# Kernel optimization log

Measured on AMD Instinct MI355X. Metric: run time of the kernel, lower is better.

Reference implementation:

```python
import jax, jax.numpy as jnp
import numpy as np
from jax import lax

NUM_SKETCH = 3
BN_EPS = 1e-5


def setup_inputs() -> dict:
    key = jax.random.key(0)
    ks = jax.random.split(key, 8)
    B, C, H, W = 32, 128, 64, 64
    D = C // 4  # comp_rate = 4
    k = 3
    x = jax.random.normal(ks[0], (B, C, H, W), dtype=jnp.float32)
    fan = C * k * k
    w1 = jax.random.normal(ks[1], (C, C, k, k), dtype=jnp.float32) / np.sqrt(fan)
    w2 = jax.random.normal(ks[2], (C, C, k, k), dtype=jnp.float32) / np.sqrt(fan)
    gamma1 = jnp.ones((C,), jnp.float32); beta1 = jnp.zeros((C,), jnp.float32)
    gamma2 = jnp.ones((C,), jnp.float32); beta2 = jnp.zeros((C,), jnp.float32)
    # count-sketch hash matrices: hs[j] is (D, C), each column c has a single 1
    idx = jax.random.randint(ks[3], (NUM_SKETCH, C), 0, D)
    hs = jax.nn.one_hot(idx, D, dtype=jnp.float32).transpose(0, 2, 1)  # (3, D, C)
    ss = (jax.random.randint(ks[4], (NUM_SKETCH, C), 0, 2) * 2 - 1).astype(jnp.float32)  # (3, C) signs
    return {"x": x, "w1": w1, "w2": w2, "gamma1": gamma1, "beta1": beta1,
            "gamma2": gamma2, "beta2": beta2, "hs": hs, "ss": ss}


def _sketch_conv_unsketch(x, w, hs, ss):
    # w: (Co, Ci, k, k); hs: (J, D, Co); ss: (J, Co)
    Co, Ci, k, _ = w.shape
    J, D, _ = hs.shape
    B, _, H, W = x.shape
    wf = w.reshape(Co, -1)  # (Co, M)
    # sketched weights per sketch j: h_j @ (wf * s_j[:, None])
    w_sk = jnp.einsum('jdc,jc,cm->jdm', hs, ss, wf).reshape(J * D, Ci, k, k)
    # one conv with J*D output channels (padding=1, stride=1 hardcoded in source)
    y = lax.conv_general_dilated(x, w_sk, window_strides=(1, 1),
                                 padding=[(1, 1), (1, 1)],
                                 dimension_numbers=('NCHW', 'OIHW', 'NCHW'))
    y = y.reshape(B, J, D, H, W)
    # unsketch activations: h_j^T @ y_j, then sign scale (num_s=1 so inner median is identity)
    y_un = jnp.einsum('jdc,bjdhw->jbchw', hs, y) * ss[:, None, :, None, None]
    return jnp.median(y_un, axis=0)  # median over the 3 sketches -> (B, Co, H, W)


def _bn_relu(y, gamma, beta):
    # BatchNorm2d in training mode: biased batch stats over (N, H, W)
    mean = jnp.mean(y, axis=(0, 2, 3), keepdims=True)
    var = jnp.var(y, axis=(0, 2, 3), keepdims=True)
    yhat = (y - mean) * lax.rsqrt(var + BN_EPS)
    return jax.nn.relu(yhat * gamma[None, :, None, None] + beta[None, :, None, None])


def reference(x, w1, w2, gamma1, beta1, gamma2, beta2, hs, ss):
    residual = x
    out1 = _bn_relu(_sketch_conv_unsketch(x, w1, hs, ss), gamma1, beta1)
    del out1  # faithful to source bug: second conv loop uses x, discarding out1
    out = _bn_relu(_sketch_conv_unsketch(x, w2, hs, ss), gamma2, beta2)
    return out + residual
```

## Files before the change

### kernel.cpp

```cpp
#include <hip/hip_runtime.h>
#include <stdint.h>

typedef __bf16 bf16x8 __attribute__((ext_vector_type(8)));
typedef float  f32x4  __attribute__((ext_vector_type(4)));

static constexpr int Bn = 32, Cn = 128, Hn = 64, Wn = 64, HWn = 4096;
static constexpr size_t OFF_XT    = 0;
static constexpr size_t OFF_WF    = 33554432;
static constexpr size_t OFF_IDX   = 33775616;
static constexpr size_t OFF_M     = 33777152;
static constexpr size_t OFF_STATS = 67331584;
static constexpr size_t OFF_ZERO  = 67347968;

__device__ __forceinline__ unsigned short f32_to_bf16(float f) {
    union { float f; unsigned u; } v; v.f = f;
    unsigned u = v.u;
    return (unsigned short)((u + 0x7FFFu + ((u >> 16) & 1u)) >> 16);
}
__device__ __forceinline__ float bf16_to_f32(unsigned short h) {
    union { unsigned u; float f; } v; v.u = ((unsigned)h) << 16;
    return v.f;
}
__device__ __forceinline__ float bf_lo(unsigned w) {
    union { unsigned u; float f; } v; v.u = w << 16; return v.f;
}
__device__ __forceinline__ float bf_hi(unsigned w) {
    union { unsigned u; float f; } v; v.u = w & 0xffff0000u; return v.f;
}
__device__ __forceinline__ float med3(float z0, float z1, float z2) {
    float lo = fminf(z0, z1), hi = fmaxf(z0, z1);
    return fmaxf(lo, fminf(hi, z2));
}
__device__ __forceinline__ void gload_lds16(const unsigned short* g, unsigned short* l) {
    __builtin_amdgcn_global_load_lds(
        (const __attribute__((address_space(1))) unsigned int*)(const void*)g,
        (__attribute__((address_space(3))) unsigned int*)(void*)l,
        16, 0, 0);
}

__global__ __launch_bounds__(256) void k_prep(const float* __restrict__ x,
                                              unsigned short* __restrict__ xT,
                                              const float* __restrict__ w2,
                                              const float* __restrict__ hs,
                                              const float* __restrict__ ss,
                                              unsigned short* __restrict__ wf,
                                              int* __restrict__ idx,
                                              float* __restrict__ stats16,
                                              float* __restrict__ zerop) {
    __shared__ __align__(16) unsigned char smraw[20480];
    int t = threadIdx.x;
    if (blockIdx.x < 432) {
        int*   idxs = (int*)smraw;
        float* sss  = (float*)(smraw + 1536);
        for (int i = t; i < 384; i += 256) {
            int j = i >> 7, c = i & 127;
            int found = 0;
#pragma unroll
            for (int d = 0; d < 32; ++d)
                if (hs[(j * 32 + d) * 128 + c] > 0.5f) found = d;
            idxs[i] = found;
            sss[i]  = ss[i];
        }
        __syncthreads();
        int f = blockIdx.x * 256 + t;
        int jj   = f & 7;
        int lane = (f >> 3) & 63;
        int nt   = (f >> 9) % 6;
        int qt   = f / (512 * 6);
        int tp   = qt % 9;
        int q    = qt / 9;
        int k  = ((lane >> 4) << 3) + jj;
        int ci = q * 32 + k;
        int n  = nt * 16 + (lane & 15);
        int j = n >> 5, d = n & 31;
        const int*   ij = idxs + j * 128;
        const float* sj = sss  + j * 128;
        float sum = 0.f;
        for (int c = 0; c < 128; ++c)
            if (ij[c] == d) sum += sj[c] * w2[(c * 128 + ci) * 9 + tp];
        wf[f] = f32_to_bf16(sum);
    } else if (blockIdx.x == 432) {
        for (int i = t; i < 384; i += 256) {
            int j = i >> 7, c = i & 127;
            int found = 0;
            for (int d = 0; d < 32; ++d)
                if (hs[(j * 32 + d) * 128 + c] > 0.5f) found = d;
            idx[i] = found;
        }
        for (int i = t; i < 4096; i += 256) stats16[i] = 0.f;
        if (t < 32) zerop[t] = 0.f;
    } else {
        unsigned short* sm = (unsigned short*)smraw;
        int blk = blockIdx.x - 433;
        int pt = blk & 15, q = (blk >> 4) & 3, b = blk >> 6;
        int p0 = pt * 256;
        const float* xp = x + ((size_t)(b * Cn + q * 32) * HWn) + p0 + t;
#pragma unroll
        for (int cil = 0; cil < 32; ++cil)
            sm[t * 40 + cil] = f32_to_bf16(xp[(size_t)cil * HWn]);
        __syncthreads();
        uint4* dst = (uint4*)(xT + ((size_t)(b * 4 + q) * HWn + p0) * 32);
#pragma unroll
        for (int pass = 0; pass < 4; ++pass) {
            int pix = pass * 64 + (t >> 2);
            int ch  = t & 3;
            dst[pix * 4 + ch] = *(const uint4*)(&sm[pix * 40 + ch * 8]);
        }
    }
}

__global__ __launch_bounds__(256, 2) void k_conv(const unsigned short* __restrict__ xT,
                                                 const unsigned short* __restrict__ wf,
                                                 const int* __restrict__ idx,
                                                 const float* __restrict__ ss,
                                                 unsigned short* __restrict__ m_out,
                                                 float* __restrict__ stats16,
                                                 const unsigned short* __restrict__ zerop) {
    __shared__ __align__(16) unsigned short sm[25344];
    __shared__ int   idx_sh[384];
    __shared__ float ss_sh[384];
    int tid  = threadIdx.x;
    int blk  = blockIdx.x;
    int tile = blk & 15, b = blk >> 4;
    int ty0  = tile * 4;
    int wv   = tid >> 6, lane = tid & 63;
    int quad = lane >> 4, l15 = lane & 15;

    for (int i = tid; i < 384; i += 256) { idx_sh[i] = idx[i]; ss_sh[i] = ss[i]; }

    int goff[7];
#pragma unroll
    for (int i = 0; i < 7; ++i) {
        int k = (i < 6) ? (tid + i * 256) : (tid + 1536);
        bool act = (i < 6) || (tid < 48);
        int r  = k >> 2;
        int cl = (k & 3) ^ ((r >> 1) & 3);
        int hy = r / 66, hx = r - hy * 66;
        int gy = ty0 + hy - 1, gx = hx - 1;
        goff[i] = (act && gy >= 0 && gy < 64 && gx >= 0 && gx < 64)
                ? ((gy * 64 + gx) * 32 + cl * 8) : -1;
    }

    f32x4 acc[4][6];
#pragma unroll
    for (int a = 0; a < 4; ++a)
#pragma unroll
        for (int nb = 0; nb < 6; ++nb) acc[a][nb] = (f32x4){0.f, 0.f, 0.f, 0.f};

    const unsigned short* wl = wf + lane * 8;

    {
        const unsigned short* xq = xT + (size_t)(b * 4) * (HWn * 32);
#pragma unroll
        for (int i = 0; i < 6; ++i) {
            int k = tid + i * 256;
            gload_lds16((goff[i] >= 0) ? (xq + goff[i]) : zerop, &sm[k * 8]);
        }
        if (tid < 48) {
            int k = tid + 1536;
            gload_lds16((goff[6] >= 0) ? (xq + goff[6]) : zerop, &sm[k * 8]);
        }
    }
    __syncthreads();

    for (int q = 0; q < 4; ++q) {
        unsigned short* cur = sm + (q & 1) * 12672;
        if (q < 3) {
            const unsigned short* xq = xT + (size_t)(b * 4 + q + 1) * (HWn * 32);
            unsigned short* nxt = sm + ((q + 1) & 1) * 12672;
#pragma unroll
            for (int i = 0; i < 6; ++i) {
                int k = tid + i * 256;
                gload_lds16((goff[i] >= 0) ? (xq + goff[i]) : zerop, &nxt[k * 8]);
            }
            if (tid < 48) {
                int k = tid + 1536;
                gload_lds16((goff[6] >= 0) ? (xq + goff[6]) : zerop, &nxt[k * 8]);
            }
        }
#pragma unroll
        for (int tp = 0; tp < 9; ++tp) {
            int dy = tp / 3, dx = tp % 3;
            bf16x8 bfr[6];
            const unsigned short* wb = wl + (size_t)((q * 9 + tp) * 6) * 512;
#pragma unroll
            for (int nb = 0; nb < 6; ++nb)
                bfr[nb] = *(const bf16x8*)(wb + nb * 512);
            bf16x8 afr[4];
#pragma unroll
            for (int mq = 0; mq < 4; ++mq) {
                int pix = (wv + dy) * 66 + mq * 16 + l15 + dx;
                int byo = (pix << 6) + (quad << 4);
                byo ^= ((byo >> 7) & 3) << 4;
                afr[mq] = *(const bf16x8*)((const unsigned char*)cur + byo);
            }
#pragma unroll
            for (int mq = 0; mq < 4; ++mq)
#pragma unroll
                for (int nb = 0; nb < 6; ++nb)
                    acc[mq][nb] = __builtin_amdgcn_mfma_f32_16x16x32_bf16(afr[mq], bfr[nb], acc[mq][nb], 0, 0, 0);
        }
        __syncthreads();
    }

#pragma unroll
    for (int mq = 0; mq < 4; ++mq)
#pragma unroll
        for (int nb = 0; nb < 6; ++nb) {
            int ch = nb * 16 + l15;
            int px = wv * 64 + mq * 16 + quad * 4;
            ushort4 v;
            v.x = f32_to_bf16(acc[mq][nb][0]);
            v.y = f32_to_bf16(acc[mq][nb][1]);
            v.z = f32_to_bf16(acc[mq][nb][2]);
            v.w = f32_to_bf16(acc[mq][nb][3]);
            *(ushort4*)(&sm[ch * 264 + px]) = v;
        }
    __syncthreads();
    int half = lane >> 5, p8 = lane & 31;
    unsigned short* mpb = m_out + (size_t)b * Cn * HWn + tile * 256 + p8 * 8;
    float* stp = stats16 + (blk & 15) * 256;
#pragma unroll 2
    for (int i = 0; i < 16; ++i) {
        int c = wv * 32 + i * 2 + half;
        int r0 = idx_sh[c], r1 = 32 + idx_sh[128 + c], r2 = 64 + idx_sh[256 + c];
        float sg0 = ss_sh[c], sg1 = ss_sh[128 + c], sg2 = ss_sh[256 + c];
        uint4 w0 = *(const uint4*)(&sm[r0 * 264 + p8 * 8]);
        uint4 w1 = *(const uint4*)(&sm[r1 * 264 + p8 * 8]);
        uint4 w2v = *(const uint4*)(&sm[r2 * 264 + p8 * 8]);
        const unsigned* u0 = (const unsigned*)&w0;
        const unsigned* u1 = (const unsigned*)&w1;
        const unsigned* u2 = (const unsigned*)&w2v;
        uint4 R;
        unsigned* rw = (unsigned*)&R;
        float s = 0.f, s2 = 0.f;
#pragma unroll
        for (int e = 0; e < 4; ++e) {
            float mlo = med3(sg0 * bf_lo(u0[e]), sg1 * bf_lo(u1[e]), sg2 * bf_lo(u2[e]));
            float mhi = med3(sg0 * bf_hi(u0[e]), sg1 * bf_hi(u1[e]), sg2 * bf_hi(u2[e]));
            s  += mlo + mhi;
            s2 += mlo * mlo + mhi * mhi;
            rw[e] = (unsigned)f32_to_bf16(mlo) | ((unsigned)f32_to_bf16(mhi) << 16);
        }
        *(uint4*)(mpb + (size_t)c * HWn) = R;
#pragma unroll
        for (int o = 16; o > 0; o >>= 1) { s += __shfl_xor(s, o); s2 += __shfl_xor(s2, o); }
        if ((lane & 31) == 0) { atomicAdd(&stp[c], s); atomicAdd(&stp[128 + c], s2); }
    }
}

__global__ __launch_bounds__(256) void k_apply(const unsigned short* __restrict__ m,
                                               const float* __restrict__ x,
                                               const float* __restrict__ stats16,
                                               const float* __restrict__ gamma,
                                               const float* __restrict__ beta,
                                               float* __restrict__ out) {
    __shared__ float co[2];
    int tid = threadIdx.x;
    int i4 = blockIdx.x * 256 + tid;
    int c = (blockIdx.x >> 2) & 127;
    if (tid < 32) {
        float v = stats16[(tid & 15) * 256 + ((tid >> 4) << 7) + c];
#pragma unroll
        for (int o = 8; o > 0; o >>= 1) v += __shfl_xor(v, o);
        if ((tid & 15) == 0) co[tid >> 4] = v;
    }
    __syncthreads();
    const float N = 131072.f;
    float mean = co[0] / N;
    float var  = co[1] / N - mean * mean;
    float sc   = gamma[c] * rsqrtf(var + 1e-5f);
    float sh   = beta[c] - mean * sc;
    ushort4 mv = ((const ushort4*)m)[i4];
    float4  xv = ((const float4*)x)[i4];
    float4 o;
    o.x = fmaxf(bf16_to_f32(mv.x) * sc + sh, 0.f) + xv.x;
    o.y = fmaxf(bf16_to_f32(mv.y) * sc + sh, 0.f) + xv.y;
    o.z = fmaxf(bf16_to_f32(mv.z) * sc + sh, 0.f) + xv.z;
    o.w = fmaxf(bf16_to_f32(mv.w) * sc + sh, 0.f) + xv.w;
    ((float4*)out)[i4] = o;
}

extern "C" void kernel_launch(void* const* d_in, const int* in_sizes, int n_in,
                              void* d_out, int out_size, void* d_ws, size_t ws_size,
                              hipStream_t stream) {
    const float* x      = (const float*)d_in[0];
    const float* w2     = (const float*)d_in[2];
    const float* gamma2 = (const float*)d_in[5];
    const float* beta2  = (const float*)d_in[6];
    const float* hs     = (const float*)d_in[7];
    const float* ss     = (const float*)d_in[8];
    float* out = (float*)d_out;

    char* ws = (char*)d_ws;
    unsigned short* xT  = (unsigned short*)(ws + OFF_XT);
    unsigned short* wfp = (unsigned short*)(ws + OFF_WF);
    int*            idp = (int*)(ws + OFF_IDX);
    unsigned short* mp  = (unsigned short*)(ws + OFF_M);
    float*          st  = (float*)(ws + OFF_STATS);
    float*          zp  = (float*)(ws + OFF_ZERO);

    k_prep<<<2481, 256, 0, stream>>>(x, xT, w2, hs, ss, wfp, idp, st, zp);
    k_conv<<<512, 256, 0, stream>>>(xT, wfp, idp, ss, mp, st, (const unsigned short*)zp);
    k_apply<<<16384, 256, 0, stream>>>(mp, x, st, gamma2, beta2, out);
}
```

Baseline: 191.9 us.

## Stage conv weights in LDS per channel quarter and drop input double buffering

Each channel quarter's sketched weights are now loaded into LDS with async global-to-LDS copies, and the MFMA B fragments are read from LDS instead of straight from global memory. To fit this, the input tile goes from double buffering to single buffering, so loads for the next quarter no longer overlap compute and each quarter gets an extra barrier. The idx and ss tables are read from global instead of shared memory. LDS rises to about 80KB per block, which with launch bounds of 2 blocks may still fit but leaves less room for occupancy.

```diff
diff --git a/kernel.cpp b/kernel.cpp
--- a/kernel.cpp
+++ b/kernel.cpp
@@ -116,17 +116,13 @@
                                                  unsigned short* __restrict__ m_out,
                                                  float* __restrict__ stats16,
                                                  const unsigned short* __restrict__ zerop) {
-    __shared__ __align__(16) unsigned short sm[25344];
-    __shared__ int   idx_sh[384];
-    __shared__ float ss_sh[384];
+    __shared__ __align__(16) unsigned short sm[40320];
     int tid  = threadIdx.x;
     int blk  = blockIdx.x;
     int tile = blk & 15, b = blk >> 4;
     int ty0  = tile * 4;
     int wv   = tid >> 6, lane = tid & 63;
     int quad = lane >> 4, l15 = lane & 15;
-
-    for (int i = tid; i < 384; i += 256) { idx_sh[i] = idx[i]; ss_sh[i] = ss[i]; }
 
     int goff[7];
 #pragma unroll
@@ -147,52 +143,48 @@
 #pragma unroll
         for (int nb = 0; nb < 6; ++nb) acc[a][nb] = (f32x4){0.f, 0.f, 0.f, 0.f};
 
-    const unsigned short* wl = wf + lane * 8;
-
-    {
-        const unsigned short* xq = xT + (size_t)(b * 4) * (HWn * 32);
-#pragma unroll
-        for (int i = 0; i < 6; ++i) {
-            int k = tid + i * 256;
-            gload_lds16((goff[i] >= 0) ? (xq + goff[i]) : zerop, &sm[k * 8]);
-        }
-        if (tid < 48) {
-            int k = tid + 1536;
-            gload_lds16((goff[6] >= 0) ? (xq + goff[6]) : zerop, &sm[k * 8]);
-        }
-    }
+#define STAGE_Q(qv)                                                                  \
+    {                                                                                \
+        const unsigned short* xq = xT + (size_t)(b * 4 + (qv)) * (HWn * 32);         \
+        _Pragma("unroll")                                                            \
+        for (int i = 0; i < 6; ++i) {                                                \
+            int k = tid + i * 256;                                                   \
+            gload_lds16((goff[i] >= 0) ? (xq + goff[i]) : zerop, &sm[k * 8]);        \
+        }                                                                            \
+        if (tid < 48) {                                                              \
+            int k = tid + 1536;                                                      \
+            gload_lds16((goff[6] >= 0) ? (xq + goff[6]) : zerop, &sm[k * 8]);        \
+        }                                                                            \
+        const unsigned short* wq = wf + (size_t)(qv) * 27648;                        \
+        _Pragma("unroll")                                                            \
+        for (int i = 0; i < 13; ++i) {                                               \
+            int k = tid + i * 256;                                                   \
+            gload_lds16(wq + k * 8, &sm[12672 + k * 8]);                             \
+        }                                                                            \
+        if (tid < 128) {                                                             \
+            int k = tid + 3328;                                                      \
+            gload_lds16(wq + k * 8, &sm[12672 + k * 8]);                             \
+        }                                                                            \
+    }
+
+    STAGE_Q(0)
     __syncthreads();
 
     for (int q = 0; q < 4; ++q) {
-        unsigned short* cur = sm + (q & 1) * 12672;
-        if (q < 3) {
-            const unsigned short* xq = xT + (size_t)(b * 4 + q + 1) * (HWn * 32);
-            unsigned short* nxt = sm + ((q + 1) & 1) * 12672;
-#pragma unroll
-            for (int i = 0; i < 6; ++i) {
-                int k = tid + i * 256;
-                gload_lds16((goff[i] >= 0) ? (xq + goff[i]) : zerop, &nxt[k * 8]);
-            }
-            if (tid < 48) {
-                int k = tid + 1536;
-                gload_lds16((goff[6] >= 0) ? (xq + goff[6]) : zerop, &nxt[k * 8]);
-            }
-        }
 #pragma unroll
         for (int tp = 0; tp < 9; ++tp) {
             int dy = tp / 3, dx = tp % 3;
             bf16x8 bfr[6];
-            const unsigned short* wb = wl + (size_t)((q * 9 + tp) * 6) * 512;
 #pragma unroll
             for (int nb = 0; nb < 6; ++nb)
-                bfr[nb] = *(const bf16x8*)(wb + nb * 512);
+                bfr[nb] = *(const bf16x8*)(&sm[12672 + (tp * 6 + nb) * 512 + lane * 8]);
             bf16x8 afr[4];
 #pragma unroll
             for (int mq = 0; mq < 4; ++mq) {
                 int pix = (wv + dy) * 66 + mq * 16 + l15 + dx;
                 int byo = (pix << 6) + (quad << 4);
                 byo ^= ((byo >> 7) & 3) << 4;
-                afr[mq] = *(const bf16x8*)((const unsigned char*)cur + byo);
+                afr[mq] = *(const bf16x8*)((const unsigned char*)sm + byo);
             }
 #pragma unroll
             for (int mq = 0; mq < 4; ++mq)
@@ -201,7 +193,12 @@
                     acc[mq][nb] = __builtin_amdgcn_mfma_f32_16x16x32_bf16(afr[mq], bfr[nb], acc[mq][nb], 0, 0, 0);
         }
         __syncthreads();
-    }
+        if (q < 3) {
+            STAGE_Q(q + 1)
+            __syncthreads();
+        }
+    }
+#undef STAGE_Q
 
 #pragma unroll
     for (int mq = 0; mq < 4; ++mq)
@@ -223,8 +220,8 @@
 #pragma unroll 2
     for (int i = 0; i < 16; ++i) {
         int c = wv * 32 + i * 2 + half;
-        int r0 = idx_sh[c], r1 = 32 + idx_sh[128 + c], r2 = 64 + idx_sh[256 + c];
-        float sg0 = ss_sh[c], sg1 = ss_sh[128 + c], sg2 = ss_sh[256 + c];
+        int r0 = idx[c], r1 = 32 + idx[128 + c], r2 = 64 + idx[256 + c];
+        float sg0 = ss[c], sg1 = ss[128 + c], sg2 = ss[256 + c];
         uint4 w0 = *(const uint4*)(&sm[r0 * 264 + p8 * 8]);
         uint4 w1 = *(const uint4*)(&sm[r1 * 264 + p8 * 8]);
         uint4 w2v = *(const uint4*)(&sm[r2 * 264 + p8 * 8]);
```

Result: no change. 194.2 us (+1.2%).

## Give each wave a private halo buffer and drop block barriers from conv loop

Applied to the files above, without the earlier changes.

Each wave now loads its own 3-row halo slice of the input into a private LDS region, so the block-wide double buffer and its per-chunk __syncthreads are replaced by a per-wave vmcnt wait. MFMA sections are wrapped in s_setprio to favour matrix issue, and the idx/ss tables are read straight from global memory instead of being staged in LDS. This removes cross-wave barrier stalls, but it also drops the prefetch overlap: loads for the next channel chunk now sit on the critical path. Because neighbouring waves need the same halo rows, each input row is also loaded redundantly, up to three times.

```diff
diff --git a/kernel.cpp b/kernel.cpp
--- a/kernel.cpp
+++ b/kernel.cpp
@@ -117,8 +117,6 @@
                                                  float* __restrict__ stats16,
                                                  const unsigned short* __restrict__ zerop) {
     __shared__ __align__(16) unsigned short sm[25344];
-    __shared__ int   idx_sh[384];
-    __shared__ float ss_sh[384];
     int tid  = threadIdx.x;
     int blk  = blockIdx.x;
     int tile = blk & 15, b = blk >> 4;
@@ -126,20 +124,7 @@
     int wv   = tid >> 6, lane = tid & 63;
     int quad = lane >> 4, l15 = lane & 15;
 
-    for (int i = tid; i < 384; i += 256) { idx_sh[i] = idx[i]; ss_sh[i] = ss[i]; }
-
-    int goff[7];
-#pragma unroll
-    for (int i = 0; i < 7; ++i) {
-        int k = (i < 6) ? (tid + i * 256) : (tid + 1536);
-        bool act = (i < 6) || (tid < 48);
-        int r  = k >> 2;
-        int cl = (k & 3) ^ ((r >> 1) & 3);
-        int hy = r / 66, hx = r - hy * 66;
-        int gy = ty0 + hy - 1, gx = hx - 1;
-        goff[i] = (act && gy >= 0 && gy < 64 && gx >= 0 && gx < 64)
-                ? ((gy * 64 + gx) * 32 + cl * 8) : -1;
-    }
+    unsigned short* priv = sm + wv * 6336;
 
     f32x4 acc[4][6];
 #pragma unroll
@@ -149,35 +134,29 @@
 
     const unsigned short* wl = wf + lane * 8;
 
-    {
-        const unsigned short* xq = xT + (size_t)(b * 4) * (HWn * 32);
-#pragma unroll
-        for (int i = 0; i < 6; ++i) {
-            int k = tid + i * 256;
-            gload_lds16((goff[i] >= 0) ? (xq + goff[i]) : zerop, &sm[k * 8]);
-        }
-        if (tid < 48) {
-            int k = tid + 1536;
-            gload_lds16((goff[6] >= 0) ? (xq + goff[6]) : zerop, &sm[k * 8]);
-        }
-    }
-    __syncthreads();
+#define STAGE_W(qv)                                                                   \
+    {                                                                                 \
+        const unsigned short* xq = xT + (size_t)(b * 4 + (qv)) * (HWn * 32);          \
+        _Pragma("unroll")                                                             \
+        for (int i = 0; i < 13; ++i) {                                                \
+            if (i < 12 || lane < 24) {                                                \
+                int k  = i * 64 + lane;                                               \
+                int r  = k >> 2;                                                      \
+                int cl = (k & 3) ^ ((r >> 1) & 3);                                    \
+                int dyl = r / 66, hx = r - dyl * 66;                                  \
+                int gy = ty0 + wv + dyl - 1, gx = hx - 1;                             \
+                const unsigned short* src =                                           \
+                    (gy >= 0 && gy < 64 && gx >= 0 && gx < 64)                        \
+                        ? (xq + ((gy * 64 + gx) * 32 + cl * 8)) : zerop;              \
+                gload_lds16(src, priv + i * 512);                                     \
+            }                                                                         \
+        }                                                                             \
+    }
+
+    STAGE_W(0)
+    asm volatile("s_waitcnt vmcnt(0)" ::: "memory");
 
     for (int q = 0; q < 4; ++q) {
-        unsigned short* cur = sm + (q & 1) * 12672;
-        if (q < 3) {
-            const unsigned short* xq = xT + (size_t)(b * 4 + q + 1) * (HWn * 32);
-            unsigned short* nxt = sm + ((q + 1) & 1) * 12672;
-#pragma unroll
-            for (int i = 0; i < 6; ++i) {
-                int k = tid + i * 256;
-                gload_lds16((goff[i] >= 0) ? (xq + goff[i]) : zerop, &nxt[k * 8]);
-            }
-            if (tid < 48) {
-                int k = tid + 1536;
-                gload_lds16((goff[6] >= 0) ? (xq + goff[6]) : zerop, &nxt[k * 8]);
-            }
-        }
 #pragma unroll
         for (int tp = 0; tp < 9; ++tp) {
             int dy = tp / 3, dx = tp % 3;
@@ -189,20 +168,26 @@
             bf16x8 afr[4];
 #pragma unroll
             for (int mq = 0; mq < 4; ++mq) {
-                int pix = (wv + dy) * 66 + mq * 16 + l15 + dx;
-                int byo = (pix << 6) + (quad << 4);
+                int byo = ((dy * 66) + mq * 16 + l15 + dx) * 64 + quad * 16;
                 byo ^= ((byo >> 7) & 3) << 4;
-                afr[mq] = *(const bf16x8*)((const unsigned char*)cur + byo);
+                afr[mq] = *(const bf16x8*)((const unsigned char*)priv + byo);
             }
+            __builtin_amdgcn_s_setprio(1);
 #pragma unroll
             for (int mq = 0; mq < 4; ++mq)
 #pragma unroll
                 for (int nb = 0; nb < 6; ++nb)
                     acc[mq][nb] = __builtin_amdgcn_mfma_f32_16x16x32_bf16(afr[mq], bfr[nb], acc[mq][nb], 0, 0, 0);
-        }
-        __syncthreads();
-    }
-
+            __builtin_amdgcn_s_setprio(0);
+        }
+        if (q < 3) {
+            STAGE_W(q + 1)
+            asm volatile("s_waitcnt vmcnt(0)" ::: "memory");
+        }
+    }
+#undef STAGE_W
+
+    __syncthreads();
 #pragma unroll
     for (int mq = 0; mq < 4; ++mq)
 #pragma unroll
@@ -223,8 +208,8 @@
 #pragma unroll 2
     for (int i = 0; i < 16; ++i) {
         int c = wv * 32 + i * 2 + half;
-        int r0 = idx_sh[c], r1 = 32 + idx_sh[128 + c], r2 = 64 + idx_sh[256 + c];
-        float sg0 = ss_sh[c], sg1 = ss_sh[128 + c], sg2 = ss_sh[256 + c];
+        int r0 = idx[c], r1 = 32 + idx[128 + c], r2 = 64 + idx[256 + c];
+        float sg0 = ss[c], sg1 = ss[128 + c], sg2 = ss[256 + c];
         uint4 w0 = *(const uint4*)(&sm[r0 * 264 + p8 * 8]);
         uint4 w1 = *(const uint4*)(&sm[r1 * 264 + p8 * 8]);
         uint4 w2v = *(const uint4*)(&sm[r2 * 264 + p8 * 8]);
```

New measurement: 197.3 us. +2.8%, slower.
